# Kernel tuning notes

Hardware: AMD Instinct MI355X
Metric: run time of the kernel (lower is better)

Reference implementation:

```python
import jax, jax.numpy as jnp
import numpy as np

B, C, H, Wd = 16, 256, 64, 64
D_MODEL = 256


def setup_inputs() -> dict:
    key = jax.random.key(0)
    kx, kw = jax.random.split(key)
    x = jax.random.normal(kx, (B, C, H, Wd), dtype=jnp.float32)
    # 1x1 conv weight [out_c=1+2*d_model, in_c], scaled like kaiming-ish init
    W = jax.random.normal(kw, (1 + 2 * D_MODEL, C), dtype=jnp.float32) / np.sqrt(C)
    return {"x": x, "W": W}


def reference(x, W):
    b, c, h, w = x.shape
    d = (W.shape[0] - 1) // 2
    n = h * w
    xf = x.reshape(b, c, n)                      # [b, c, N]
    qkv = jnp.einsum('oc,bcn->bon', W, xf)       # 1x1 conv == channel GEMM
    q = qkv[:, :1]                               # [b, 1, N]
    k = qkv[:, 1:1 + d]                          # [b, d, N]
    v = qkv[:, 1 + d:]                           # [b, d, N]
    scores = jax.nn.softmax(q, axis=-1)          # softmax over tokens
    ctx = jnp.sum(k * scores, axis=-1, keepdims=True)  # [b, d, 1]
    out = jax.nn.relu(v) * ctx                   # gated ReLU(v)
    return out.reshape(b, d, h, w)
```

## Files before the change

kernel.cpp:

```cpp
#include <hip/hip_runtime.h>
#include <cstdint>
#include <cstddef>

#define NB 16
#define NC 256
#define NN 4096
#define ND 256

typedef unsigned short u16;
typedef unsigned int u32;

typedef __attribute__((ext_vector_type(8))) short short8;
typedef __attribute__((ext_vector_type(4))) float f32x4;

__device__ __forceinline__ u16 f2bf(float f) {
  union { float f; u32 u; } v; v.f = f;
  u32 r = v.u + 0x7FFFu + ((v.u >> 16) & 1u);
  return (u16)(r >> 16);
}
__device__ __forceinline__ float bf2f(u16 h) {
  union { u32 u; float f; } v; v.u = ((u32)h) << 16; return v.f;
}

__global__ __launch_bounds__(256) void k_zero(float* __restrict__ q,
                                              float* __restrict__ xs) {
  const int i = blockIdx.x * 256 + threadIdx.x;
  if (i < NB * NN) q[i] = 0.f;
  else xs[i - NB * NN] = 0.f;
}

__global__ __launch_bounds__(256) void k_cast_transpose_q(const float* __restrict__ x,
                                                          const float* __restrict__ W,
                                                          u16* __restrict__ xbT,
                                                          float* __restrict__ q) {
  __shared__ __align__(16) u16 tile[64 * 68];
  __shared__ float qred[16 * 64];
  const int t = threadIdx.x;
  const int b = blockIdx.z, c0 = blockIdx.y * 64, n0 = blockIdx.x * 64;
  const float* xb = x + (size_t)(b * NC + c0) * NN + n0;
  const int nl = (t & 15) * 4;
  float qacc[4] = {0.f, 0.f, 0.f, 0.f};
#pragma unroll
  for (int i = 0; i < 4; ++i) {
    int cl = (t >> 4) + i * 16;
    float4 v = *(const float4*)(xb + (size_t)cl * NN + nl);
    const float wq = W[c0 + cl];
    qacc[0] += wq * v.x; qacc[1] += wq * v.y;
    qacc[2] += wq * v.z; qacc[3] += wq * v.w;
    tile[(nl + 0) * 68 + cl] = f2bf(v.x);
    tile[(nl + 1) * 68 + cl] = f2bf(v.y);
    tile[(nl + 2) * 68 + cl] = f2bf(v.z);
    tile[(nl + 3) * 68 + cl] = f2bf(v.w);
  }
#pragma unroll
  for (int j = 0; j < 4; ++j) qred[(t >> 4) * 64 + nl + j] = qacc[j];
  __syncthreads();
  u16* ob = xbT + (size_t)(b * NN + n0) * NC + c0;
#pragma unroll
  for (int i = 0; i < 4; ++i) {
    int e = t + i * 256;
    int rn = e >> 4;
    int rc = (e & 15) * 4;
    ushort4 pv = *(const ushort4*)&tile[rn * 68 + rc];
    *(ushort4*)(ob + (size_t)rn * NC + rc) = pv;
  }
  if (t < 64) {
    float s = 0.f;
#pragma unroll
    for (int k = 0; k < 16; ++k) s += qred[k * 64 + t];
    atomicAdd(&q[b * NN + n0 + t], s);
  }
}

__global__ __launch_bounds__(256) void k_softmax(const float* __restrict__ q,
                                                 float* __restrict__ s) {
  __shared__ float red[256];
  const int b = blockIdx.x, t = threadIdx.x;
  const float* qb = q + b * NN;
  float v[16];
  float m = -3.4e38f;
#pragma unroll
  for (int i = 0; i < 16; ++i) { v[i] = qb[t + i * 256]; m = fmaxf(m, v[i]); }
  red[t] = m;
  __syncthreads();
  for (int off = 128; off > 0; off >>= 1) {
    if (t < off) red[t] = fmaxf(red[t], red[t + off]);
    __syncthreads();
  }
  const float M = red[0];
  __syncthreads();
  float sum = 0.f;
#pragma unroll
  for (int i = 0; i < 16; ++i) { v[i] = __expf(v[i] - M); sum += v[i]; }
  red[t] = sum;
  __syncthreads();
  for (int off = 128; off > 0; off >>= 1) {
    if (t < off) red[t] += red[t + off];
    __syncthreads();
  }
  const float inv = 1.f / red[0];
  float* sb = s + b * NN;
#pragma unroll
  for (int i = 0; i < 16; ++i) sb[t + i * 256] = v[i] * inv;
}

__global__ __launch_bounds__(256) void k_xs(const u16* __restrict__ xbT,
                                            const float* __restrict__ s,
                                            float* __restrict__ xs) {
  const int t = threadIdx.x;
  const int b = blockIdx.y, n0 = blockIdx.x * 128;
  const u16* xp = xbT + ((size_t)(b * NN + n0)) * NC + t;
  const float* sp = s + b * NN + n0;
  float acc = 0.f;
#pragma unroll 8
  for (int j = 0; j < 128; ++j) {
    acc += bf2f(xp[(size_t)j * NC]) * sp[j];
  }
  atomicAdd(&xs[b * NC + t], acc);
}

__global__ __launch_bounds__(256) void k_ctx(const float* __restrict__ W,
                                             const float* __restrict__ xs,
                                             float* __restrict__ ctx) {
  __shared__ float sx[NC];
  const int b = blockIdx.x, d = threadIdx.x;
  sx[d] = xs[b * NC + d];
  __syncthreads();
  const float* wk = W + (size_t)(1 + d) * NC;
  float acc = 0.f;
#pragma unroll 4
  for (int c = 0; c < NC; ++c) acc += wk[c] * sx[c];
  ctx[b * NC + d] = acc;
}

__global__ __launch_bounds__(256) void k_castwv(const float* __restrict__ W,
                                                u16* __restrict__ wvb) {
  const int i = (blockIdx.x * 256 + threadIdx.x) * 4;
  const float4 v = *(const float4*)(W + (size_t)(1 + ND) * NC + i);
  ushort4 o;
  o.x = f2bf(v.x); o.y = f2bf(v.y); o.z = f2bf(v.z); o.w = f2bf(v.w);
  *(ushort4*)(wvb + i) = o;
}

#define BM 128
#define BN 128
#define BK 64

__global__ __launch_bounds__(256) void k_gemm(const u16* __restrict__ xbT,
                                              const u16* __restrict__ wvb,
                                              const float* __restrict__ ctx,
                                              float* __restrict__ out) {
  __shared__ __align__(16) u16 As[BM * BK];
  __shared__ __align__(16) u16 Bs[BN * BK];
  const int t = threadIdx.x;
  const int b = blockIdx.z;
  const int d0 = blockIdx.y * BM;
  const int n0 = blockIdx.x * BN;
  const int lane = t & 63, w = t >> 6;
  const int wd = (w & 1) * 64, wn = (w >> 1) * 64;
  const int quad = lane >> 4, l15 = lane & 15;

  f32x4 acc[4][4];
#pragma unroll
  for (int mi = 0; mi < 4; ++mi)
#pragma unroll
    for (int ni = 0; ni < 4; ++ni)
      acc[mi][ni] = (f32x4){0.f, 0.f, 0.f, 0.f};

  const int rstg = t >> 3;
  const int l8 = (((t & 7) ^ (rstg & 7))) * 8;
  const u16* gA = wvb + (size_t)(d0 + rstg) * NC + l8;
  const u16* gB = xbT + (size_t)(b * NN + n0 + rstg) * NC + l8;
  const int ldst = 8 * t;

  const int pq0 = ((0 * 4 + quad) ^ (l15 & 7)) * 8;
  const int pq1 = ((1 * 4 + quad) ^ (l15 & 7)) * 8;

  for (int kk = 0; kk < NC; kk += BK) {
    __syncthreads();
#pragma unroll
    for (int i = 0; i < 4; ++i) {
      __builtin_amdgcn_global_load_lds(
          (const __attribute__((address_space(1))) u32*)(gA + kk + (size_t)(32 * i) * NC),
          (__attribute__((address_space(3))) u32*)(As + 2048 * i + ldst), 16, 0, 0);
      __builtin_amdgcn_global_load_lds(
          (const __attribute__((address_space(1))) u32*)(gB + kk + (size_t)(32 * i) * NC),
          (__attribute__((address_space(3))) u32*)(Bs + 2048 * i + ldst), 16, 0, 0);
    }
    __syncthreads();

#pragma unroll
    for (int kq = 0; kq < 2; ++kq) {
      const int pq = kq ? pq1 : pq0;
      short8 af[4], bfr[4];
#pragma unroll
      for (int mi = 0; mi < 4; ++mi)
        af[mi] = *(const short8*)&As[(wd + mi * 16 + l15) * BK + pq];
#pragma unroll
      for (int ni = 0; ni < 4; ++ni)
        bfr[ni] = *(const short8*)&Bs[(wn + ni * 16 + l15) * BK + pq];
#pragma unroll
      for (int mi = 0; mi < 4; ++mi)
#pragma unroll
        for (int ni = 0; ni < 4; ++ni)
          acc[mi][ni] = __builtin_amdgcn_mfma_f32_16x16x32_bf16(af[mi], bfr[ni],
                                                                acc[mi][ni], 0, 0, 0);
    }
  }

#pragma unroll
  for (int mi = 0; mi < 4; ++mi) {
#pragma unroll
    for (int r = 0; r < 4; ++r) {
      const int d = d0 + wd + mi * 16 + quad * 4 + r;
      const float cx = ctx[b * NC + d];
      float* op = out + (size_t)(b * NC + d) * NN + n0 + wn + l15;
#pragma unroll
      for (int ni = 0; ni < 4; ++ni) {
        float v = acc[mi][ni][r];
        op[ni * 16] = fmaxf(v, 0.f) * cx;
      }
    }
  }
}

extern "C" void kernel_launch(void* const* d_in, const int* in_sizes, int n_in,
                              void* d_out, int out_size, void* d_ws, size_t ws_size,
                              hipStream_t stream) {
  const float* x = (const float*)d_in[0];
  const float* W = (const float*)d_in[1];
  float* out = (float*)d_out;

  char* ws = (char*)d_ws;
  u16* xbT   = (u16*)ws;
  float* q   = (float*)(ws + 33554432);
  float* s   = (float*)(ws + 33554432 + 262144);
  float* xs  = (float*)(ws + 33554432 + 524288);
  float* ctx = (float*)(ws + 33554432 + 540672);
  u16* wvb   = (u16*)(ws + 33554432 + 557056);

  k_zero<<<272, 256, 0, stream>>>(q, xs);
  k_cast_transpose_q<<<dim3(64, 4, 16), 256, 0, stream>>>(x, W, xbT, q);
  k_softmax<<<16, 256, 0, stream>>>(q, s);
  k_xs<<<dim3(32, 16), 256, 0, stream>>>(xbT, s, xs);
  k_ctx<<<16, 256, 0, stream>>>(W, xs, ctx);
  k_castwv<<<64, 256, 0, stream>>>(W, wvb);
  k_gemm<<<dim3(32, 2, 16), 256, 0, stream>>>(xbT, wvb, ctx, out);
}
```

Measured before the change: 154.2 us.

## Fuse init kernels, widen softmax and xs reductions, load GEMM fragments directly

Merges the zeroing and Wv bf16 cast into one init launch, removing a kernel launch. Softmax now uses 1024 threads with float4 loads and wave shuffles, and the xs reduction uses vectorized ushort4 loads with a shared-memory combine. The GEMM drops LDS staging and loads MFMA fragments straight from global memory with register double-buffering, using 64x256 tiles. This removes LDS traffic and barriers, but operands are no longer shared through LDS, so global/L2 traffic rises and the row-strided fragment loads may coalesce poorly.

```diff
diff --git a/kernel.cpp b/kernel.cpp
--- a/kernel.cpp
+++ b/kernel.cpp
@@ -22,11 +22,22 @@
   union { u32 u; float f; } v; v.u = ((u32)h) << 16; return v.f;
 }
 
-__global__ __launch_bounds__(256) void k_zero(float* __restrict__ q,
-                                              float* __restrict__ xs) {
-  const int i = blockIdx.x * 256 + threadIdx.x;
-  if (i < NB * NN) q[i] = 0.f;
-  else xs[i - NB * NN] = 0.f;
+__global__ __launch_bounds__(256) void k_init(const float* __restrict__ W,
+                                              float* __restrict__ q,
+                                              float* __restrict__ xs,
+                                              u16* __restrict__ wvb) {
+  const int blk = blockIdx.x, t = threadIdx.x;
+  if (blk < 272) {
+    const int i = blk * 256 + t;
+    if (i < NB * NN) q[i] = 0.f;
+    else xs[i - NB * NN] = 0.f;
+  } else {
+    const int i = ((blk - 272) * 256 + t) * 4;
+    const float4 v = *(const float4*)(W + (size_t)(1 + ND) * NC + i);
+    ushort4 o;
+    o.x = f2bf(v.x); o.y = f2bf(v.y); o.z = f2bf(v.z); o.w = f2bf(v.w);
+    *(ushort4*)(wvb + i) = o;
+  }
 }
 
 __global__ __launch_bounds__(256) void k_cast_transpose_q(const float* __restrict__ x,
@@ -72,51 +83,59 @@
   }
 }
 
-__global__ __launch_bounds__(256) void k_softmax(const float* __restrict__ q,
-                                                 float* __restrict__ s) {
-  __shared__ float red[256];
+__global__ __launch_bounds__(1024) void k_softmax(const float* __restrict__ q,
+                                                  float* __restrict__ s) {
+  __shared__ float redm[16];
+  __shared__ float redz[16];
   const int b = blockIdx.x, t = threadIdx.x;
-  const float* qb = q + b * NN;
-  float v[16];
-  float m = -3.4e38f;
-#pragma unroll
-  for (int i = 0; i < 16; ++i) { v[i] = qb[t + i * 256]; m = fmaxf(m, v[i]); }
-  red[t] = m;
-  __syncthreads();
-  for (int off = 128; off > 0; off >>= 1) {
-    if (t < off) red[t] = fmaxf(red[t], red[t + off]);
-    __syncthreads();
-  }
-  const float M = red[0];
-  __syncthreads();
-  float sum = 0.f;
-#pragma unroll
-  for (int i = 0; i < 16; ++i) { v[i] = __expf(v[i] - M); sum += v[i]; }
-  red[t] = sum;
-  __syncthreads();
-  for (int off = 128; off > 0; off >>= 1) {
-    if (t < off) red[t] += red[t + off];
-    __syncthreads();
-  }
-  const float inv = 1.f / red[0];
-  float* sb = s + b * NN;
-#pragma unroll
-  for (int i = 0; i < 16; ++i) sb[t + i * 256] = v[i] * inv;
+  const int wave = t >> 6, lane = t & 63;
+  float4 v = *(const float4*)(q + (size_t)b * NN + t * 4);
+  float m = fmaxf(fmaxf(v.x, v.y), fmaxf(v.z, v.w));
+#pragma unroll
+  for (int off = 32; off > 0; off >>= 1) m = fmaxf(m, __shfl_down(m, off));
+  if (lane == 0) redm[wave] = m;
+  __syncthreads();
+  float M = redm[0];
+#pragma unroll
+  for (int k = 1; k < 16; ++k) M = fmaxf(M, redm[k]);
+  float4 e;
+  e.x = __expf(v.x - M); e.y = __expf(v.y - M);
+  e.z = __expf(v.z - M); e.w = __expf(v.w - M);
+  float sum = e.x + e.y + e.z + e.w;
+#pragma unroll
+  for (int off = 32; off > 0; off >>= 1) sum += __shfl_down(sum, off);
+  if (lane == 0) redz[wave] = sum;
+  __syncthreads();
+  float Z = 0.f;
+#pragma unroll
+  for (int k = 0; k < 16; ++k) Z += redz[k];
+  const float inv = 1.f / Z;
+  e.x *= inv; e.y *= inv; e.z *= inv; e.w *= inv;
+  *(float4*)(s + (size_t)b * NN + t * 4) = e;
 }
 
 __global__ __launch_bounds__(256) void k_xs(const u16* __restrict__ xbT,
                                             const float* __restrict__ s,
                                             float* __restrict__ xs) {
+  __shared__ float red[4 * 256];
   const int t = threadIdx.x;
   const int b = blockIdx.y, n0 = blockIdx.x * 128;
-  const u16* xp = xbT + ((size_t)(b * NN + n0)) * NC + t;
-  const float* sp = s + b * NN + n0;
-  float acc = 0.f;
+  const int w = t >> 6, c4 = (t & 63) * 4;
+  const u16* xp = xbT + ((size_t)(b * NN + n0 + w * 32)) * NC + c4;
+  const float* sp = s + b * NN + n0 + w * 32;
+  float a0 = 0.f, a1 = 0.f, a2 = 0.f, a3 = 0.f;
 #pragma unroll 8
-  for (int j = 0; j < 128; ++j) {
-    acc += bf2f(xp[(size_t)j * NC]) * sp[j];
-  }
-  atomicAdd(&xs[b * NC + t], acc);
+  for (int j = 0; j < 32; ++j) {
+    ushort4 v = *(const ushort4*)(xp + (size_t)j * NC);
+    float sv = sp[j];
+    a0 += bf2f(v.x) * sv; a1 += bf2f(v.y) * sv;
+    a2 += bf2f(v.z) * sv; a3 += bf2f(v.w) * sv;
+  }
+  red[w * 256 + c4 + 0] = a0; red[w * 256 + c4 + 1] = a1;
+  red[w * 256 + c4 + 2] = a2; red[w * 256 + c4 + 3] = a3;
+  __syncthreads();
+  float sum = red[t] + red[256 + t] + red[512 + t] + red[768 + t];
+  atomicAdd(&xs[b * NC + t], sum);
 }
 
 __global__ __launch_bounds__(256) void k_ctx(const float* __restrict__ W,
@@ -133,32 +152,20 @@
   ctx[b * NC + d] = acc;
 }
 
-__global__ __launch_bounds__(256) void k_castwv(const float* __restrict__ W,
-                                                u16* __restrict__ wvb) {
-  const int i = (blockIdx.x * 256 + threadIdx.x) * 4;
-  const float4 v = *(const float4*)(W + (size_t)(1 + ND) * NC + i);
-  ushort4 o;
-  o.x = f2bf(v.x); o.y = f2bf(v.y); o.z = f2bf(v.z); o.w = f2bf(v.w);
-  *(ushort4*)(wvb + i) = o;
-}
-
-#define BM 128
-#define BN 128
-#define BK 64
-
 __global__ __launch_bounds__(256) void k_gemm(const u16* __restrict__ xbT,
                                               const u16* __restrict__ wvb,
                                               const float* __restrict__ ctx,
                                               float* __restrict__ out) {
-  __shared__ __align__(16) u16 As[BM * BK];
-  __shared__ __align__(16) u16 Bs[BN * BK];
   const int t = threadIdx.x;
   const int b = blockIdx.z;
-  const int d0 = blockIdx.y * BM;
-  const int n0 = blockIdx.x * BN;
+  const int d0 = blockIdx.y * 64;
+  const int n0 = blockIdx.x * 256;
   const int lane = t & 63, w = t >> 6;
-  const int wd = (w & 1) * 64, wn = (w >> 1) * 64;
+  const int wn = w * 64;
   const int quad = lane >> 4, l15 = lane & 15;
+
+  const u16* pA = wvb + (size_t)(d0 + l15) * NC + quad * 8;
+  const u16* pB = xbT + (size_t)(b * NN + n0 + wn + l15) * NC + quad * 8;
 
   f32x4 acc[4][4];
 #pragma unroll
@@ -167,52 +174,41 @@
     for (int ni = 0; ni < 4; ++ni)
       acc[mi][ni] = (f32x4){0.f, 0.f, 0.f, 0.f};
 
-  const int rstg = t >> 3;
-  const int l8 = (((t & 7) ^ (rstg & 7))) * 8;
-  const u16* gA = wvb + (size_t)(d0 + rstg) * NC + l8;
-  const u16* gB = xbT + (size_t)(b * NN + n0 + rstg) * NC + l8;
-  const int ldst = 8 * t;
-
-  const int pq0 = ((0 * 4 + quad) ^ (l15 & 7)) * 8;
-  const int pq1 = ((1 * 4 + quad) ^ (l15 & 7)) * 8;
-
-  for (int kk = 0; kk < NC; kk += BK) {
-    __syncthreads();
-#pragma unroll
-    for (int i = 0; i < 4; ++i) {
-      __builtin_amdgcn_global_load_lds(
-          (const __attribute__((address_space(1))) u32*)(gA + kk + (size_t)(32 * i) * NC),
-          (__attribute__((address_space(3))) u32*)(As + 2048 * i + ldst), 16, 0, 0);
-      __builtin_amdgcn_global_load_lds(
-          (const __attribute__((address_space(1))) u32*)(gB + kk + (size_t)(32 * i) * NC),
-          (__attribute__((address_space(3))) u32*)(Bs + 2048 * i + ldst), 16, 0, 0);
-    }
-    __syncthreads();
-
-#pragma unroll
-    for (int kq = 0; kq < 2; ++kq) {
-      const int pq = kq ? pq1 : pq0;
-      short8 af[4], bfr[4];
-#pragma unroll
-      for (int mi = 0; mi < 4; ++mi)
-        af[mi] = *(const short8*)&As[(wd + mi * 16 + l15) * BK + pq];
+  short8 af[2][4], bfr[2][4];
+#pragma unroll
+  for (int mi = 0; mi < 4; ++mi) af[0][mi] = *(const short8*)(pA + (size_t)mi * 16 * NC);
+#pragma unroll
+  for (int ni = 0; ni < 4; ++ni) bfr[0][ni] = *(const short8*)(pB + (size_t)ni * 16 * NC);
+
+#pragma unroll
+  for (int kt = 1; kt < 8; ++kt) {
+    const int cur = (kt - 1) & 1, nxt = kt & 1;
+    const int kk = kt * 32;
+#pragma unroll
+    for (int mi = 0; mi < 4; ++mi)
+      af[nxt][mi] = *(const short8*)(pA + (size_t)mi * 16 * NC + kk);
+#pragma unroll
+    for (int ni = 0; ni < 4; ++ni)
+      bfr[nxt][ni] = *(const short8*)(pB + (size_t)ni * 16 * NC + kk);
+#pragma unroll
+    for (int mi = 0; mi < 4; ++mi)
 #pragma unroll
       for (int ni = 0; ni < 4; ++ni)
-        bfr[ni] = *(const short8*)&Bs[(wn + ni * 16 + l15) * BK + pq];
-#pragma unroll
-      for (int mi = 0; mi < 4; ++mi)
-#pragma unroll
-        for (int ni = 0; ni < 4; ++ni)
-          acc[mi][ni] = __builtin_amdgcn_mfma_f32_16x16x32_bf16(af[mi], bfr[ni],
-                                                                acc[mi][ni], 0, 0, 0);
-    }
-  }
+        acc[mi][ni] = __builtin_amdgcn_mfma_f32_16x16x32_bf16(af[cur][mi], bfr[cur][ni],
+                                                              acc[mi][ni], 0, 0, 0);
+  }
+#pragma unroll
+  for (int mi = 0; mi < 4; ++mi)
+#pragma unroll
+    for (int ni = 0; ni < 4; ++ni)
+      acc[mi][ni] = __builtin_amdgcn_mfma_f32_16x16x32_bf16(af[1][mi], bfr[1][ni],
+                                                            acc[mi][ni], 0, 0, 0);
 
 #pragma unroll
   for (int mi = 0; mi < 4; ++mi) {
 #pragma unroll
     for (int r = 0; r < 4; ++r) {
-      const int d = d0 + wd + mi * 16 + quad * 4 + r;
+      const int d = d0 + mi * 16 + quad * 4 + r;
       const float cx = ctx[b * NC + d];
       float* op = out + (size_t)(b * NC + d) * NN + n0 + wn + l15;
 #pragma unroll
@@ -239,11 +235,10 @@
   float* ctx = (float*)(ws + 33554432 + 540672);
   u16* wvb   = (u16*)(ws + 33554432 + 557056);
 
-  k_zero<<<272, 256, 0, stream>>>(q, xs);
+  k_init<<<336, 256, 0, stream>>>(W, q, xs, wvb);
   k_cast_transpose_q<<<dim3(64, 4, 16), 256, 0, stream>>>(x, W, xbT, q);
-  k_softmax<<<16, 256, 0, stream>>>(q, s);
+  k_softmax<<<16, 1024, 0, stream>>>(q, s);
   k_xs<<<dim3(32, 16), 256, 0, stream>>>(xbT, s, xs);
   k_ctx<<<16, 256, 0, stream>>>(W, xs, ctx);
-  k_castwv<<<64, 256, 0, stream>>>(W, wvb);
-  k_gemm<<<dim3(32, 2, 16), 256, 0, stream>>>(xbT, wvb, ctx, out);
-}
+  k_gemm<<<dim3(16, 4, 16), 256, 0, stream>>>(xbT, wvb, ctx, out);
+}
```

Measured after the change: 169.1 us. 1.1x slower.
